# Kernel tuning notes

Hardware: AMD Instinct MI355X
Metric: run time of the kernel (lower is better)

The kernel has to match this reference:

```python
import jax, jax.numpy as jnp
import numpy as np

DIM = 1024
HEAD_NUM = 8
D_HEAD = DIM // HEAD_NUM
B, S = 4, 2048


def setup_inputs() -> dict:
    key = jax.random.key(0)
    ks = jax.random.split(key, 7)
    scale = 0.02
    return {
        "Q": jax.random.normal(ks[0], (B, S, DIM), dtype=jnp.float32),
        "K": jax.random.normal(ks[1], (B, S, DIM), dtype=jnp.float32),
        "V": jax.random.normal(ks[2], (B, S, DIM), dtype=jnp.float32),
        "W_Q": jax.random.normal(ks[3], (DIM, DIM), dtype=jnp.float32) * scale,
        "W_K": jax.random.normal(ks[4], (DIM, DIM), dtype=jnp.float32) * scale,
        "W_V": jax.random.normal(ks[5], (DIM, DIM), dtype=jnp.float32) * scale,
        "W_O": jax.random.normal(ks[6], (DIM, DIM), dtype=jnp.float32) * scale,
    }


def reference(Q, K, V, W_Q, W_K, W_V, W_O):
    # torch nn.Linear(bias=False): y = x @ W.T
    b, s, d = Q.shape
    h, dh = HEAD_NUM, d // HEAD_NUM

    def proj_split(x, W):
        # split_head: tensor_split along feature dim into h contiguous chunks,
        # stack at dim 1 -> [b, h, s, dh]; equivalent to reshape+transpose.
        y = jnp.einsum('bsd,ed->bse', x, W)
        return y.reshape(b, s, h, dh).transpose(0, 2, 1, 3)

    q = proj_split(Q, W_Q)  # [b,h,s,dh]
    k = proj_split(K, W_K)
    v = proj_split(V, W_V)

    scores = jnp.einsum('bhqd,bhkd->bhqk', q, k) / jnp.sqrt(jnp.float32(dh))
    # FAITHFUL to original: nn.Softmax(dim=1) normalizes over the HEAD axis.
    attn = jax.nn.softmax(scores, axis=1)
    # dropout is identity in eval mode
    ctx = jnp.einsum('bhqk,bhkd->bhqd', attn, v)  # [b,h,s,dh]
    # concat_head: heads concatenated back along feature dim in order
    ctx = ctx.transpose(0, 2, 1, 3).reshape(b, s, d)
    return jnp.einsum('bsd,ed->bse', ctx, W_O)
```

## Files before the change

### kernel.cpp

```cpp
#include <hip/hip_runtime.h>
#include <math.h>
#include <stdint.h>


typedef __attribute__((ext_vector_type(8))) __bf16 bf16x8;
typedef __attribute__((ext_vector_type(4))) __bf16 bf16x4;
typedef __attribute__((ext_vector_type(4))) float  f32x4;

__device__ __forceinline__ f32x4 mfma16(bf16x8 a, bf16x8 b, f32x4 c) {
    return __builtin_amdgcn_mfma_f32_16x16x32_bf16(a, b, c, 0, 0, 0);
}

__device__ __forceinline__ void cp16(void* lds, const void* g) {
    __builtin_amdgcn_global_load_lds(
        (__attribute__((address_space(1))) void*)(void*)(const_cast<void*>(g)),
        (__attribute__((address_space(3))) void*)lds,
        16, 0, 0);
}

__global__ void cast_f32_to_bf16(const float* __restrict__ src,
                                 __bf16* __restrict__ dst, int n4) {
    int i = blockIdx.x * blockDim.x + threadIdx.x;
    const int stride = gridDim.x * blockDim.x;
    for (; i < n4; i += stride) {
        float4 f = ((const float4*)src)[i];
        bf16x4 o;
        o[0] = (__bf16)f.x; o[1] = (__bf16)f.y; o[2] = (__bf16)f.z; o[3] = (__bf16)f.w;
        ((bf16x4*)dst)[i] = o;
    }
}

__global__ void cast4_f32_to_bf16(const float* __restrict__ s0, __bf16* __restrict__ d0,
                                  const float* __restrict__ s1, __bf16* __restrict__ d1,
                                  const float* __restrict__ s2, __bf16* __restrict__ d2,
                                  const float* __restrict__ s3, __bf16* __restrict__ d3,
                                  int n4) {
    const float* s = (blockIdx.y == 0) ? s0 : (blockIdx.y == 1) ? s1
                    : (blockIdx.y == 2) ? s2 : s3;
    __bf16* d = (blockIdx.y == 0) ? d0 : (blockIdx.y == 1) ? d1
               : (blockIdx.y == 2) ? d2 : d3;
    int i = blockIdx.x * blockDim.x + threadIdx.x;
    const int stride = gridDim.x * blockDim.x;
    for (; i < n4; i += stride) {
        float4 f = ((const float4*)s)[i];
        bf16x4 o;
        o[0] = (__bf16)f.x; o[1] = (__bf16)f.y; o[2] = (__bf16)f.z; o[3] = (__bf16)f.w;
        ((bf16x4*)d)[i] = o;
    }
}

template<int MODE>
__global__ __launch_bounds__(256, 2) void gemm_bt(const __bf16* __restrict__ A,
                                                  const __bf16* __restrict__ Bt,
                                                  void* __restrict__ out,
                                                  float scale)
{
    __shared__ __bf16 As[128 * 32];
    __shared__ __bf16 Bs[128 * 32];
    const int tid  = threadIdx.x;
    const int lane = tid & 63;
    const int u = lane >> 4, v = lane & 15;
    const int w = tid >> 6;
    const int wm = (w >> 1) * 64, wn = (w & 1) * 64;
    const long tM = (long)blockIdx.y * 128;
    const int  tN = blockIdx.x * 128;

    f32x4 acc[4][4];
#pragma unroll
    for (int i = 0; i < 4; ++i)
#pragma unroll
        for (int j = 0; j < 4; ++j) acc[i][j] = (f32x4){0.f, 0.f, 0.f, 0.f};

    const int c0 = tid, c1 = tid + 256;
    const int ar0 = c0 >> 2, ak0 = (c0 & 3) * 8;
    const int ar1 = c1 >> 2, ak1 = (c1 & 3) * 8;

    const __bf16* Ab = A  + tM * 1024;
    const __bf16* Bb = Bt + (long)tN * 1024;

    for (int k0 = 0; k0 < 1024; k0 += 32) {
        __syncthreads();
        cp16(&As[ar0 * 32 + ak0], Ab + (long)ar0 * 1024 + k0 + ak0);
        cp16(&As[ar1 * 32 + ak1], Ab + (long)ar1 * 1024 + k0 + ak1);
        cp16(&Bs[ar0 * 32 + ak0], Bb + (long)ar0 * 1024 + k0 + ak0);
        cp16(&Bs[ar1 * 32 + ak1], Bb + (long)ar1 * 1024 + k0 + ak1);
        __syncthreads();

        bf16x8 af[4], bfr[4];
#pragma unroll
        for (int i = 0; i < 4; ++i)
            af[i] = *(const bf16x8*)&As[(wm + i * 16 + v) * 32 + u * 8];
#pragma unroll
        for (int j = 0; j < 4; ++j)
            bfr[j] = *(const bf16x8*)&Bs[(wn + j * 16 + v) * 32 + u * 8];
#pragma unroll
        for (int i = 0; i < 4; ++i)
#pragma unroll
            for (int j = 0; j < 4; ++j)
                acc[i][j] = mfma16(af[i], bfr[j], acc[i][j]);
    }

#pragma unroll
    for (int i = 0; i < 4; ++i) {
#pragma unroll
        for (int j = 0; j < 4; ++j) {
            const long row0 = tM + wm + i * 16 + u * 4;
            const int  col  = tN + wn + j * 16 + v;
            if (MODE == 0) {
                __bf16* o = (__bf16*)out;
#pragma unroll
                for (int r = 0; r < 4; ++r)
                    o[(row0 + r) * 1024 + col] = (__bf16)(acc[i][j][r] * scale);
            } else if (MODE == 1) {
                float* o = (float*)out;
#pragma unroll
                for (int r = 0; r < 4; ++r)
                    o[(row0 + r) * 1024 + col] = acc[i][j][r];
            } else {
                __bf16* o = (__bf16*)out;
                const int bidx = (int)(row0 >> 11);
                const int s    = (int)(row0 & 2047);
                const int h = col >> 7, dh = col & 127;
                bf16x4 pk;
#pragma unroll
                for (int r = 0; r < 4; ++r) pk[r] = (__bf16)acc[i][j][r];
                *(bf16x4*)&o[((long)(bidx * 8 + h) * 128 + dh) * 2048 + s] = pk;
            }
        }
    }
}

__global__ __launch_bounds__(256, 4) void qk_head_softmax(
    const __bf16* __restrict__ kp, const __bf16* __restrict__ qp,
    __bf16* __restrict__ P, int b_base, int q_base)
{
    __shared__ __bf16 As[64 * 32];
    __shared__ __bf16 Bs[128 * 32];
    __shared__ __bf16 tb[128 * 68];
    const int tid  = threadIdx.x;
    const int lane = tid & 63;
    const int u = lane >> 4, v = lane & 15;
    const int w = tid >> 6;
    const int wm = (w >> 1) * 32, wn = (w & 1) * 64;
    const int bloc = blockIdx.z;
    const int b    = b_base + bloc;
    const int k0   = blockIdx.x * 64;
    const int q0l  = blockIdx.y * 128;
    const int q0g  = q_base + q0l;
    const long Cq  = (long)gridDim.y * 128;

    const int ar0 = tid >> 2, ak0 = (tid & 3) * 8;
    const int ar1 = ar0 + 64, ak1 = ak0;

    const __bf16* Ka = kp + ((long)b * 2048 + k0) * 1024;
    const __bf16* Qa = qp + ((long)b * 2048 + q0g) * 1024;

    f32x4 den[2][4];
#pragma unroll
    for (int i = 0; i < 2; ++i)
#pragma unroll
        for (int j = 0; j < 4; ++j) den[i][j] = (f32x4){0.f, 0.f, 0.f, 0.f};

#pragma unroll 1
    for (int h = 0; h < 8; ++h) {
        f32x4 acc[2][4];
#pragma unroll
        for (int i = 0; i < 2; ++i)
#pragma unroll
            for (int j = 0; j < 4; ++j) acc[i][j] = (f32x4){0.f, 0.f, 0.f, 0.f};

#pragma unroll
        for (int kb = 0; kb < 4; ++kb) {
            const int co = h * 128 + kb * 32;
            __syncthreads();
            cp16(&As[ar0 * 32 + ak0], Ka + (long)ar0 * 1024 + co + ak0);
            cp16(&Bs[ar0 * 32 + ak0], Qa + (long)ar0 * 1024 + co + ak0);
            cp16(&Bs[ar1 * 32 + ak1], Qa + (long)ar1 * 1024 + co + ak1);
            __syncthreads();

            bf16x8 af[2], bfr[4];
#pragma unroll
            for (int i = 0; i < 2; ++i)
                af[i] = *(const bf16x8*)&As[(wm + i * 16 + v) * 32 + u * 8];
#pragma unroll
            for (int j = 0; j < 4; ++j)
                bfr[j] = *(const bf16x8*)&Bs[(wn + j * 16 + v) * 32 + u * 8];
#pragma unroll
            for (int i = 0; i < 2; ++i)
#pragma unroll
                for (int j = 0; j < 4; ++j)
                    acc[i][j] = mfma16(af[i], bfr[j], acc[i][j]);
        }
#pragma unroll
        for (int i = 0; i < 2; ++i)
#pragma unroll
            for (int j = 0; j < 4; ++j)
#pragma unroll
                for (int r = 0; r < 4; ++r)
                    den[i][j][r] += __expf(acc[i][j][r]);
    }

#pragma unroll
    for (int i = 0; i < 2; ++i)
#pragma unroll
        for (int j = 0; j < 4; ++j)
#pragma unroll
            for (int r = 0; r < 4; ++r) den[i][j][r] = 1.0f / den[i][j][r];

#pragma unroll 1
    for (int h = 0; h < 8; ++h) {
        f32x4 acc[2][4];
#pragma unroll
        for (int i = 0; i < 2; ++i)
#pragma unroll
            for (int j = 0; j < 4; ++j) acc[i][j] = (f32x4){0.f, 0.f, 0.f, 0.f};

#pragma unroll
        for (int kb = 0; kb < 4; ++kb) {
            const int co = h * 128 + kb * 32;
            __syncthreads();
            cp16(&As[ar0 * 32 + ak0], Ka + (long)ar0 * 1024 + co + ak0);
            cp16(&Bs[ar0 * 32 + ak0], Qa + (long)ar0 * 1024 + co + ak0);
            cp16(&Bs[ar1 * 32 + ak1], Qa + (long)ar1 * 1024 + co + ak1);
            __syncthreads();

            bf16x8 af[2], bfr[4];
#pragma unroll
            for (int i = 0; i < 2; ++i)
                af[i] = *(const bf16x8*)&As[(wm + i * 16 + v) * 32 + u * 8];
#pragma unroll
            for (int j = 0; j < 4; ++j)
                bfr[j] = *(const bf16x8*)&Bs[(wn + j * 16 + v) * 32 + u * 8];
#pragma unroll
            for (int i = 0; i < 2; ++i)
#pragma unroll
                for (int j = 0; j < 4; ++j)
                    acc[i][j] = mfma16(af[i], bfr[j], acc[i][j]);
        }
        __syncthreads();
#pragma unroll
        for (int i = 0; i < 2; ++i)
#pragma unroll
            for (int j = 0; j < 4; ++j) {
                const int kc = wm + i * 16 + u * 4;
                const int qr = wn + j * 16 + v;
                bf16x4 o;
#pragma unroll
                for (int r = 0; r < 4; ++r) {
                    float e = (float)(__bf16)__expf(acc[i][j][r]);
                    o[r] = (__bf16)(e * den[i][j][r]);
                }
                *(bf16x4*)&tb[qr * 68 + kc] = o;
            }
        __syncthreads();
        __bf16* Ph = P + ((long)(bloc * 8 + h) * Cq + q0l) * 2048 + k0;
#pragma unroll
        for (int p = 0; p < 4; ++p) {
            const int qq = p * 32 + (tid >> 3);
            const int kk = (tid & 7) * 8;
            *(bf16x8*)&Ph[(long)qq * 2048 + kk] = *(const bf16x8*)&tb[qq * 68 + kk];
        }
    }
}

__global__ __launch_bounds__(256, 2) void pv_gemm(
    const __bf16* __restrict__ vt, const __bf16* __restrict__ P,
    __bf16* __restrict__ ctx, int b_base, int q_base)
{
    __shared__ __bf16 As[128 * 32];
    __shared__ __bf16 Bs[128 * 32];
    const int tid  = threadIdx.x;
    const int lane = tid & 63;
    const int u = lane >> 4, v = lane & 15;
    const int w = tid >> 6;
    const int wm = (w >> 1) * 64, wn = (w & 1) * 64;
    const int bhl  = blockIdx.y;
    const int bloc = bhl >> 3, h = bhl & 7;
    const int b    = b_base + bloc;
    const int q0l  = blockIdx.x * 128;
    const int q0g  = q_base + q0l;
    const long Cq  = (long)gridDim.x * 128;

    const int c0 = tid, c1 = tid + 256;
    const int ar0 = c0 >> 2, ak0 = (c0 & 3) * 8;
    const int ar1 = c1 >> 2, ak1 = (c1 & 3) * 8;

    const __bf16* Ab = vt + (long)(b * 8 + h) * 128 * 2048;
    const __bf16* Bb = P  + ((long)(bloc * 8 + h) * Cq + q0l) * 2048;

    f32x4 acc[4][4];
#pragma unroll
    for (int i = 0; i < 4; ++i)
#pragma unroll
        for (int j = 0; j < 4; ++j) acc[i][j] = (f32x4){0.f, 0.f, 0.f, 0.f};

    for (int k0 = 0; k0 < 2048; k0 += 32) {
        __syncthreads();
        cp16(&As[ar0 * 32 + ak0], Ab + (long)ar0 * 2048 + k0 + ak0);
        cp16(&As[ar1 * 32 + ak1], Ab + (long)ar1 * 2048 + k0 + ak1);
        cp16(&Bs[ar0 * 32 + ak0], Bb + (long)ar0 * 2048 + k0 + ak0);
        cp16(&Bs[ar1 * 32 + ak1], Bb + (long)ar1 * 2048 + k0 + ak1);
        __syncthreads();

        bf16x8 af[4], bfr[4];
#pragma unroll
        for (int i = 0; i < 4; ++i)
            af[i] = *(const bf16x8*)&As[(wm + i * 16 + v) * 32 + u * 8];
#pragma unroll
        for (int j = 0; j < 4; ++j)
            bfr[j] = *(const bf16x8*)&Bs[(wn + j * 16 + v) * 32 + u * 8];
#pragma unroll
        for (int i = 0; i < 4; ++i)
#pragma unroll
            for (int j = 0; j < 4; ++j)
                acc[i][j] = mfma16(af[i], bfr[j], acc[i][j]);
    }

#pragma unroll
    for (int i = 0; i < 4; ++i) {
#pragma unroll
        for (int j = 0; j < 4; ++j) {
            const int dh0 = wm + i * 16 + u * 4;
            const int q   = q0g + wn + j * 16 + v;
            bf16x4 pk;
#pragma unroll
            for (int r = 0; r < 4; ++r) pk[r] = (__bf16)acc[i][j][r];
            *(bf16x4*)&ctx[((long)b * 2048 + q) * 1024 + h * 128 + dh0] = pk;
        }
    }
}

__global__ __launch_bounds__(256, 2) void attn_softmax_head(
    const __bf16* __restrict__ qp, const __bf16* __restrict__ kp,
    const __bf16* __restrict__ vt, __bf16* __restrict__ ctx)
{
    __shared__ float part[8 * 256];
    __shared__ float pb[4][2][16 * 33];

    const int tid  = threadIdx.x;
    const int lane = tid & 63;
    const int w = tid >> 6;
    const int u = lane >> 4, v = lane & 15;
    const int b  = blockIdx.y;
    const int q0 = blockIdx.x * 16;

    const long qoff = ((long)b * 2048 + q0 + v) * 1024;
    bf16x8 qf[2][4];
#pragma unroll
    for (int hh = 0; hh < 2; ++hh) {
        const int h = 2 * w + hh;
#pragma unroll
        for (int kk = 0; kk < 4; ++kk)
            qf[hh][kk] = *(const bf16x8*)(qp + qoff + h * 128 + kk * 32 + u * 8);
    }

    f32x4 acc[2][8];
#pragma unroll
    for (int hh = 0; hh < 2; ++hh)
#pragma unroll
        for (int dt = 0; dt < 8; ++dt) acc[hh][dt] = (f32x4){0.f, 0.f, 0.f, 0.f};

    for (int kt = 0; kt < 2048; kt += 32) {
        float e[2][2][4];
#pragma unroll
        for (int hh = 0; hh < 2; ++hh) {
            const int h = 2 * w + hh;
#pragma unroll
            for (int t = 0; t < 2; ++t) {
                f32x4 s = (f32x4){0.f, 0.f, 0.f, 0.f};
                const __bf16* kb = kp + ((long)b * 2048 + kt + t * 16 + v) * 1024
                                      + h * 128 + u * 8;
#pragma unroll
                for (int kk = 0; kk < 4; ++kk)
                    s = mfma16(*(const bf16x8*)(kb + kk * 32), qf[hh][kk], s);
#pragma unroll
                for (int r = 0; r < 4; ++r) e[hh][t][r] = __expf(s[r]);
            }
        }
#pragma unroll
        for (int t = 0; t < 2; ++t)
#pragma unroll
            for (int r = 0; r < 4; ++r)
                part[(t * 4 + r) * 256 + w * 64 + lane] = e[0][t][r] + e[1][t][r];
        __syncthreads();
#pragma unroll
        for (int t = 0; t < 2; ++t)
#pragma unroll
            for (int r = 0; r < 4; ++r) {
                const int j = (t * 4 + r) * 256 + lane;
                const float den = part[j] + part[j + 64] + part[j + 128] + part[j + 192];
                const float rinv = 1.0f / den;
                const int kl = t * 16 + u * 4 + r;
                pb[w][0][v * 33 + kl] = e[0][t][r] * rinv;
                pb[w][1][v * 33 + kl] = e[1][t][r] * rinv;
            }
        bf16x8 pf[2];
#pragma unroll
        for (int hh = 0; hh < 2; ++hh)
#pragma unroll
            for (int jj = 0; jj < 8; ++jj)
                pf[hh][jj] = (__bf16)pb[w][hh][v * 33 + u * 8 + jj];
#pragma unroll
        for (int hh = 0; hh < 2; ++hh) {
            const int h = 2 * w + hh;
            const __bf16* vb = vt + ((long)(b * 8 + h) * 128 + v) * 2048 + kt + u * 8;
#pragma unroll
            for (int dt = 0; dt < 8; ++dt)
                acc[hh][dt] = mfma16(*(const bf16x8*)(vb + (long)dt * 16 * 2048),
                                     pf[hh], acc[hh][dt]);
        }
        __syncthreads();
    }

#pragma unroll
    for (int hh = 0; hh < 2; ++hh) {
        const int h = 2 * w + hh;
#pragma unroll
        for (int dt = 0; dt < 8; ++dt) {
            bf16x4 o;
#pragma unroll
            for (int r = 0; r < 4; ++r) o[r] = (__bf16)acc[hh][dt][r];
            *(bf16x4*)(ctx + ((long)b * 2048 + q0 + v) * 1024
                           + h * 128 + dt * 16 + u * 4) = o;
        }
    }
}

extern "C" void kernel_launch(void* const* d_in, const int* in_sizes, int n_in,
                              void* d_out, int out_size, void* d_ws, size_t ws_size,
                              hipStream_t stream)
{
    const float* Q  = (const float*)d_in[0];
    const float* K  = (const float*)d_in[1];
    const float* V  = (const float*)d_in[2];
    const float* WQ = (const float*)d_in[3];
    const float* WK = (const float*)d_in[4];
    const float* WV = (const float*)d_in[5];
    const float* WO = (const float*)d_in[6];

    __bf16* ws = (__bf16*)d_ws;
    __bf16* wq = ws;
    __bf16* wk = wq + 1048576;
    __bf16* wv = wk + 1048576;
    __bf16* wo = wv + 1048576;
    __bf16* xb = wo + 1048576;
    __bf16* qp = xb + 8388608;
    __bf16* kp = qp + 8388608;
    __bf16* vt = kp + 8388608;
    __bf16* pbuf = vt + 8388608;

    const float qscale = 0.08838834764831845f;

    cast4_f32_to_bf16<<<dim3(256, 4), 256, 0, stream>>>(
        WQ, wq, WK, wk, WV, wv, WO, wo, 262144);

    dim3 gg(8, 64), gb(256);
    cast_f32_to_bf16<<<4096, 256, 0, stream>>>(Q, xb, 2097152);
    gemm_bt<0><<<gg, gb, 0, stream>>>(xb, wq, qp, qscale);
    cast_f32_to_bf16<<<4096, 256, 0, stream>>>(K, xb, 2097152);
    gemm_bt<0><<<gg, gb, 0, stream>>>(xb, wk, kp, 1.0f);
    cast_f32_to_bf16<<<4096, 256, 0, stream>>>(V, xb, 2097152);
    gemm_bt<2><<<gg, gb, 0, stream>>>(xb, wv, vt, 1.0f);

    const size_t baseBytes = 37748736ULL * 2ULL;
    const size_t avail = (ws_size > baseBytes) ? ws_size - baseBytes : 0;
    const int cfgs[6][2] = {{4,2048},{2,2048},{1,2048},{1,1024},{1,512},{1,256}};
    int nb = 0, C = 0;
    for (int c = 0; c < 6; ++c) {
        const size_t need = (size_t)cfgs[c][0] * 8 * cfgs[c][1] * 2048 * 2;
        if (need <= avail) { nb = cfgs[c][0]; C = cfgs[c][1]; break; }
    }

    if (nb) {
        for (int bb = 0; bb < 4; bb += nb)
            for (int qq = 0; qq < 2048; qq += C) {
                qk_head_softmax<<<dim3(32, C / 128, nb), gb, 0, stream>>>(
                    kp, qp, pbuf, bb, qq);
                pv_gemm<<<dim3(C / 128, nb * 8), gb, 0, stream>>>(
                    vt, pbuf, xb, bb, qq);
            }
    } else {
        attn_softmax_head<<<dim3(128, 4), gb, 0, stream>>>(qp, kp, vt, xb);
    }

    gemm_bt<1><<<gg, gb, 0, stream>>>(xb, wo, (float*)d_out, 1.0f);
}
```

Baseline: 502.1 us.

## Fuse head-axis softmax and PV into one attention kernel; batch QKV projections

Replaces the materialized probability buffer path (qk_head_softmax writing P, then pv_gemm) with a single fused_attn kernel. In it, eight waves each own one head for a 32-query tile, the softmax denominator across heads is reduced through LDS, and the normalized probabilities are fed straight into the PV MFMAs. The three input casts and the three projection GEMMs are each batched into single launches via a grid z/y dimension. This removes the large P round trip through HBM and several launches. In exchange, K and V are read directly from global memory without LDS tiling, and the kernel needs two block-wide syncs per key tile.

```diff
diff --git a/kernel.cpp b/kernel.cpp
--- a/kernel.cpp
+++ b/kernel.cpp
@@ -16,18 +16,6 @@
         (__attribute__((address_space(1))) void*)(void*)(const_cast<void*>(g)),
         (__attribute__((address_space(3))) void*)lds,
         16, 0, 0);
-}
-
-__global__ void cast_f32_to_bf16(const float* __restrict__ src,
-                                 __bf16* __restrict__ dst, int n4) {
-    int i = blockIdx.x * blockDim.x + threadIdx.x;
-    const int stride = gridDim.x * blockDim.x;
-    for (; i < n4; i += stride) {
-        float4 f = ((const float4*)src)[i];
-        bf16x4 o;
-        o[0] = (__bf16)f.x; o[1] = (__bf16)f.y; o[2] = (__bf16)f.z; o[3] = (__bf16)f.w;
-        ((bf16x4*)dst)[i] = o;
-    }
 }
 
 __global__ void cast4_f32_to_bf16(const float* __restrict__ s0, __bf16* __restrict__ d0,
@@ -49,6 +37,22 @@
     }
 }
 
+__global__ void cast3_f32_to_bf16(const float* __restrict__ s0, __bf16* __restrict__ d0,
+                                  const float* __restrict__ s1, __bf16* __restrict__ d1,
+                                  const float* __restrict__ s2, __bf16* __restrict__ d2,
+                                  int n4) {
+    const float* s = (blockIdx.y == 0) ? s0 : (blockIdx.y == 1) ? s1 : s2;
+    __bf16* d = (blockIdx.y == 0) ? d0 : (blockIdx.y == 1) ? d1 : d2;
+    int i = blockIdx.x * blockDim.x + threadIdx.x;
+    const int stride = gridDim.x * blockDim.x;
+    for (; i < n4; i += stride) {
+        float4 f = ((const float4*)s)[i];
+        bf16x4 o;
+        o[0] = (__bf16)f.x; o[1] = (__bf16)f.y; o[2] = (__bf16)f.z; o[3] = (__bf16)f.w;
+        ((bf16x4*)d)[i] = o;
+    }
+}
+
 template<int MODE>
 __global__ __launch_bounds__(256, 2) void gemm_bt(const __bf16* __restrict__ A,
                                                   const __bf16* __restrict__ Bt,
@@ -106,200 +110,64 @@
         for (int j = 0; j < 4; ++j) {
             const long row0 = tM + wm + i * 16 + u * 4;
             const int  col  = tN + wn + j * 16 + v;
-            if (MODE == 0) {
-                __bf16* o = (__bf16*)out;
-#pragma unroll
-                for (int r = 0; r < 4; ++r)
-                    o[(row0 + r) * 1024 + col] = (__bf16)(acc[i][j][r] * scale);
-            } else if (MODE == 1) {
+            if (MODE == 1) {
                 float* o = (float*)out;
 #pragma unroll
                 for (int r = 0; r < 4; ++r)
                     o[(row0 + r) * 1024 + col] = acc[i][j][r];
             } else {
                 __bf16* o = (__bf16*)out;
-                const int bidx = (int)(row0 >> 11);
-                const int s    = (int)(row0 & 2047);
-                const int h = col >> 7, dh = col & 127;
-                bf16x4 pk;
-#pragma unroll
-                for (int r = 0; r < 4; ++r) pk[r] = (__bf16)acc[i][j][r];
-                *(bf16x4*)&o[((long)(bidx * 8 + h) * 128 + dh) * 2048 + s] = pk;
+#pragma unroll
+                for (int r = 0; r < 4; ++r)
+                    o[(row0 + r) * 1024 + col] = (__bf16)(acc[i][j][r] * scale);
             }
         }
     }
 }
 
-__global__ __launch_bounds__(256, 4) void qk_head_softmax(
-    const __bf16* __restrict__ kp, const __bf16* __restrict__ qp,
-    __bf16* __restrict__ P, int b_base, int q_base)
-{
-    __shared__ __bf16 As[64 * 32];
-    __shared__ __bf16 Bs[128 * 32];
-    __shared__ __bf16 tb[128 * 68];
-    const int tid  = threadIdx.x;
-    const int lane = tid & 63;
-    const int u = lane >> 4, v = lane & 15;
-    const int w = tid >> 6;
-    const int wm = (w >> 1) * 32, wn = (w & 1) * 64;
-    const int bloc = blockIdx.z;
-    const int b    = b_base + bloc;
-    const int k0   = blockIdx.x * 64;
-    const int q0l  = blockIdx.y * 128;
-    const int q0g  = q_base + q0l;
-    const long Cq  = (long)gridDim.y * 128;
-
-    const int ar0 = tid >> 2, ak0 = (tid & 3) * 8;
-    const int ar1 = ar0 + 64, ak1 = ak0;
-
-    const __bf16* Ka = kp + ((long)b * 2048 + k0) * 1024;
-    const __bf16* Qa = qp + ((long)b * 2048 + q0g) * 1024;
-
-    f32x4 den[2][4];
-#pragma unroll
-    for (int i = 0; i < 2; ++i)
-#pragma unroll
-        for (int j = 0; j < 4; ++j) den[i][j] = (f32x4){0.f, 0.f, 0.f, 0.f};
-
-#pragma unroll 1
-    for (int h = 0; h < 8; ++h) {
-        f32x4 acc[2][4];
-#pragma unroll
-        for (int i = 0; i < 2; ++i)
-#pragma unroll
-            for (int j = 0; j < 4; ++j) acc[i][j] = (f32x4){0.f, 0.f, 0.f, 0.f};
-
-#pragma unroll
-        for (int kb = 0; kb < 4; ++kb) {
-            const int co = h * 128 + kb * 32;
-            __syncthreads();
-            cp16(&As[ar0 * 32 + ak0], Ka + (long)ar0 * 1024 + co + ak0);
-            cp16(&Bs[ar0 * 32 + ak0], Qa + (long)ar0 * 1024 + co + ak0);
-            cp16(&Bs[ar1 * 32 + ak1], Qa + (long)ar1 * 1024 + co + ak1);
-            __syncthreads();
-
-            bf16x8 af[2], bfr[4];
-#pragma unroll
-            for (int i = 0; i < 2; ++i)
-                af[i] = *(const bf16x8*)&As[(wm + i * 16 + v) * 32 + u * 8];
-#pragma unroll
-            for (int j = 0; j < 4; ++j)
-                bfr[j] = *(const bf16x8*)&Bs[(wn + j * 16 + v) * 32 + u * 8];
-#pragma unroll
-            for (int i = 0; i < 2; ++i)
-#pragma unroll
-                for (int j = 0; j < 4; ++j)
-                    acc[i][j] = mfma16(af[i], bfr[j], acc[i][j]);
-        }
-#pragma unroll
-        for (int i = 0; i < 2; ++i)
-#pragma unroll
-            for (int j = 0; j < 4; ++j)
-#pragma unroll
-                for (int r = 0; r < 4; ++r)
-                    den[i][j][r] += __expf(acc[i][j][r]);
-    }
-
-#pragma unroll
-    for (int i = 0; i < 2; ++i)
-#pragma unroll
-        for (int j = 0; j < 4; ++j)
-#pragma unroll
-            for (int r = 0; r < 4; ++r) den[i][j][r] = 1.0f / den[i][j][r];
-
-#pragma unroll 1
-    for (int h = 0; h < 8; ++h) {
-        f32x4 acc[2][4];
-#pragma unroll
-        for (int i = 0; i < 2; ++i)
-#pragma unroll
-            for (int j = 0; j < 4; ++j) acc[i][j] = (f32x4){0.f, 0.f, 0.f, 0.f};
-
-#pragma unroll
-        for (int kb = 0; kb < 4; ++kb) {
-            const int co = h * 128 + kb * 32;
-            __syncthreads();
-            cp16(&As[ar0 * 32 + ak0], Ka + (long)ar0 * 1024 + co + ak0);
-            cp16(&Bs[ar0 * 32 + ak0], Qa + (long)ar0 * 1024 + co + ak0);
-            cp16(&Bs[ar1 * 32 + ak1], Qa + (long)ar1 * 1024 + co + ak1);
-            __syncthreads();
-
-            bf16x8 af[2], bfr[4];
-#pragma unroll
-            for (int i = 0; i < 2; ++i)
-                af[i] = *(const bf16x8*)&As[(wm + i * 16 + v) * 32 + u * 8];
-#pragma unroll
-            for (int j = 0; j < 4; ++j)
-                bfr[j] = *(const bf16x8*)&Bs[(wn + j * 16 + v) * 32 + u * 8];
-#pragma unroll
-            for (int i = 0; i < 2; ++i)
-#pragma unroll
-                for (int j = 0; j < 4; ++j)
-                    acc[i][j] = mfma16(af[i], bfr[j], acc[i][j]);
-        }
-        __syncthreads();
-#pragma unroll
-        for (int i = 0; i < 2; ++i)
-#pragma unroll
-            for (int j = 0; j < 4; ++j) {
-                const int kc = wm + i * 16 + u * 4;
-                const int qr = wn + j * 16 + v;
-                bf16x4 o;
-#pragma unroll
-                for (int r = 0; r < 4; ++r) {
-                    float e = (float)(__bf16)__expf(acc[i][j][r]);
-                    o[r] = (__bf16)(e * den[i][j][r]);
-                }
-                *(bf16x4*)&tb[qr * 68 + kc] = o;
-            }
-        __syncthreads();
-        __bf16* Ph = P + ((long)(bloc * 8 + h) * Cq + q0l) * 2048 + k0;
-#pragma unroll
-        for (int p = 0; p < 4; ++p) {
-            const int qq = p * 32 + (tid >> 3);
-            const int kk = (tid & 7) * 8;
-            *(bf16x8*)&Ph[(long)qq * 2048 + kk] = *(const bf16x8*)&tb[qq * 68 + kk];
-        }
-    }
-}
-
-__global__ __launch_bounds__(256, 2) void pv_gemm(
-    const __bf16* __restrict__ vt, const __bf16* __restrict__ P,
-    __bf16* __restrict__ ctx, int b_base, int q_base)
+__global__ __launch_bounds__(256, 2) void qkv_proj(
+    const __bf16* __restrict__ xq, const __bf16* __restrict__ xk,
+    const __bf16* __restrict__ xv,
+    const __bf16* __restrict__ wq, const __bf16* __restrict__ wk,
+    const __bf16* __restrict__ wv,
+    __bf16* __restrict__ qp, __bf16* __restrict__ kp, __bf16* __restrict__ vtb,
+    float qscale)
 {
     __shared__ __bf16 As[128 * 32];
     __shared__ __bf16 Bs[128 * 32];
+    const int z = blockIdx.z;
+    const __bf16* A  = (z == 0) ? xq : (z == 1) ? xk : xv;
+    const __bf16* Bt = (z == 0) ? wq : (z == 1) ? wk : wv;
+    __bf16* out      = (z == 0) ? qp : (z == 1) ? kp : vtb;
+    const float scale = (z == 0) ? qscale : 1.0f;
+
     const int tid  = threadIdx.x;
     const int lane = tid & 63;
     const int u = lane >> 4, v = lane & 15;
     const int w = tid >> 6;
     const int wm = (w >> 1) * 64, wn = (w & 1) * 64;
-    const int bhl  = blockIdx.y;
-    const int bloc = bhl >> 3, h = bhl & 7;
-    const int b    = b_base + bloc;
-    const int q0l  = blockIdx.x * 128;
-    const int q0g  = q_base + q0l;
-    const long Cq  = (long)gridDim.x * 128;
+    const long tM = (long)blockIdx.y * 128;
+    const int  tN = blockIdx.x * 128;
+
+    f32x4 acc[4][4];
+#pragma unroll
+    for (int i = 0; i < 4; ++i)
+#pragma unroll
+        for (int j = 0; j < 4; ++j) acc[i][j] = (f32x4){0.f, 0.f, 0.f, 0.f};
 
     const int c0 = tid, c1 = tid + 256;
     const int ar0 = c0 >> 2, ak0 = (c0 & 3) * 8;
     const int ar1 = c1 >> 2, ak1 = (c1 & 3) * 8;
 
-    const __bf16* Ab = vt + (long)(b * 8 + h) * 128 * 2048;
-    const __bf16* Bb = P  + ((long)(bloc * 8 + h) * Cq + q0l) * 2048;
-
-    f32x4 acc[4][4];
-#pragma unroll
-    for (int i = 0; i < 4; ++i)
-#pragma unroll
-        for (int j = 0; j < 4; ++j) acc[i][j] = (f32x4){0.f, 0.f, 0.f, 0.f};
-
-    for (int k0 = 0; k0 < 2048; k0 += 32) {
-        __syncthreads();
-        cp16(&As[ar0 * 32 + ak0], Ab + (long)ar0 * 2048 + k0 + ak0);
-        cp16(&As[ar1 * 32 + ak1], Ab + (long)ar1 * 2048 + k0 + ak1);
-        cp16(&Bs[ar0 * 32 + ak0], Bb + (long)ar0 * 2048 + k0 + ak0);
-        cp16(&Bs[ar1 * 32 + ak1], Bb + (long)ar1 * 2048 + k0 + ak1);
+    const __bf16* Ab = A  + tM * 1024;
+    const __bf16* Bb = Bt + (long)tN * 1024;
+
+    for (int k0 = 0; k0 < 1024; k0 += 32) {
+        __syncthreads();
+        cp16(&As[ar0 * 32 + ak0], Ab + (long)ar0 * 1024 + k0 + ak0);
+        cp16(&As[ar1 * 32 + ak1], Ab + (long)ar1 * 1024 + k0 + ak1);
+        cp16(&Bs[ar0 * 32 + ak0], Bb + (long)ar0 * 1024 + k0 + ak0);
+        cp16(&Bs[ar1 * 32 + ak1], Bb + (long)ar1 * 1024 + k0 + ak1);
         __syncthreads();
 
         bf16x8 af[4], bfr[4];
@@ -320,110 +188,159 @@
     for (int i = 0; i < 4; ++i) {
 #pragma unroll
         for (int j = 0; j < 4; ++j) {
-            const int dh0 = wm + i * 16 + u * 4;
-            const int q   = q0g + wn + j * 16 + v;
-            bf16x4 pk;
-#pragma unroll
-            for (int r = 0; r < 4; ++r) pk[r] = (__bf16)acc[i][j][r];
-            *(bf16x4*)&ctx[((long)b * 2048 + q) * 1024 + h * 128 + dh0] = pk;
-        }
-    }
-}
-
-__global__ __launch_bounds__(256, 2) void attn_softmax_head(
+            const long row0 = tM + wm + i * 16 + u * 4;
+            const int  col  = tN + wn + j * 16 + v;
+            if (z < 2) {
+#pragma unroll
+                for (int r = 0; r < 4; ++r)
+                    out[(row0 + r) * 1024 + col] = (__bf16)(acc[i][j][r] * scale);
+            } else {
+                const int bidx = (int)(row0 >> 11);
+                const int s    = (int)(row0 & 2047);
+                const int h = col >> 7, dh = col & 127;
+                bf16x4 pk;
+#pragma unroll
+                for (int r = 0; r < 4; ++r) pk[r] = (__bf16)acc[i][j][r];
+                *(bf16x4*)&out[((long)(bidx * 8 + h) * 128 + dh) * 2048 + s] = pk;
+            }
+        }
+    }
+}
+
+__global__ __launch_bounds__(512, 2) void fused_attn(
     const __bf16* __restrict__ qp, const __bf16* __restrict__ kp,
     const __bf16* __restrict__ vt, __bf16* __restrict__ ctx)
 {
-    __shared__ float part[8 * 256];
-    __shared__ float pb[4][2][16 * 33];
+    __shared__ f32x4 dbuf[8][8][64];
+    __shared__ f32x4 rbuf[8][64];
+    __shared__ __bf16 Pl[8][32][64];
 
     const int tid  = threadIdx.x;
+    const int w    = tid >> 6;
     const int lane = tid & 63;
-    const int w = tid >> 6;
     const int u = lane >> 4, v = lane & 15;
-    const int b  = blockIdx.y;
-    const int q0 = blockIdx.x * 16;
-
-    const long qoff = ((long)b * 2048 + q0 + v) * 1024;
+
+    const int g0 = blockIdx.x;
+    const int xs = g0 & 7, idx = g0 >> 3;
+    const int b  = xs >> 1;
+    const int qt = idx * 2 + (xs & 1);
+    const int q0 = qt * 32;
+    const int h  = w;
+
+    const __bf16* Qb = qp + ((long)b * 2048 + q0) * 1024 + h * 128;
+    const __bf16* Kb = kp + (long)b * 2048 * 1024 + h * 128;
+    const __bf16* Vb = vt + (long)(b * 8 + h) * 128 * 2048;
+
     bf16x8 qf[2][4];
 #pragma unroll
-    for (int hh = 0; hh < 2; ++hh) {
-        const int h = 2 * w + hh;
+    for (int qj = 0; qj < 2; ++qj)
 #pragma unroll
         for (int kk = 0; kk < 4; ++kk)
-            qf[hh][kk] = *(const bf16x8*)(qp + qoff + h * 128 + kk * 32 + u * 8);
-    }
-
-    f32x4 acc[2][8];
-#pragma unroll
-    for (int hh = 0; hh < 2; ++hh)
-#pragma unroll
-        for (int dt = 0; dt < 8; ++dt) acc[hh][dt] = (f32x4){0.f, 0.f, 0.f, 0.f};
-
-    for (int kt = 0; kt < 2048; kt += 32) {
-        float e[2][2][4];
-#pragma unroll
-        for (int hh = 0; hh < 2; ++hh) {
-            const int h = 2 * w + hh;
-#pragma unroll
-            for (int t = 0; t < 2; ++t) {
-                f32x4 s = (f32x4){0.f, 0.f, 0.f, 0.f};
-                const __bf16* kb = kp + ((long)b * 2048 + kt + t * 16 + v) * 1024
-                                      + h * 128 + u * 8;
+            qf[qj][kk] = *(const bf16x8*)&Qb[(long)(qj * 16 + v) * 1024 + kk * 32 + u * 8];
+
+    f32x4 ctxa[8][2];
+#pragma unroll
+    for (int dt = 0; dt < 8; ++dt)
+#pragma unroll
+        for (int qj = 0; qj < 2; ++qj) ctxa[dt][qj] = (f32x4){0.f, 0.f, 0.f, 0.f};
+
+    for (int kt = 0; kt < 2048; kt += 64) {
+        f32x4 e[4][2];
+#pragma unroll
+        for (int ki = 0; ki < 4; ++ki)
+#pragma unroll
+            for (int qj = 0; qj < 2; ++qj) e[ki][qj] = (f32x4){0.f, 0.f, 0.f, 0.f};
+
+#pragma unroll
+        for (int ki = 0; ki < 4; ++ki) {
+            bf16x8 kf[4];
+#pragma unroll
+            for (int kk = 0; kk < 4; ++kk)
+                kf[kk] = *(const bf16x8*)&Kb[(long)(kt + ki * 16 + v) * 1024 + kk * 32 + u * 8];
+#pragma unroll
+            for (int qj = 0; qj < 2; ++qj)
 #pragma unroll
                 for (int kk = 0; kk < 4; ++kk)
-                    s = mfma16(*(const bf16x8*)(kb + kk * 32), qf[hh][kk], s);
-#pragma unroll
-                for (int r = 0; r < 4; ++r) e[hh][t][r] = __expf(s[r]);
+                    e[ki][qj] = mfma16(kf[kk], qf[qj][kk], e[ki][qj]);
+        }
+
+#pragma unroll
+        for (int ki = 0; ki < 4; ++ki)
+#pragma unroll
+            for (int qj = 0; qj < 2; ++qj)
+#pragma unroll
+                for (int r = 0; r < 4; ++r)
+                    e[ki][qj][r] = __expf(e[ki][qj][r]);
+
+        bf16x8 vf0[8];
+#pragma unroll
+        for (int dt = 0; dt < 8; ++dt)
+            vf0[dt] = *(const bf16x8*)&Vb[(long)(dt * 16 + v) * 2048 + kt + u * 8];
+
+#pragma unroll
+        for (int ki = 0; ki < 4; ++ki)
+#pragma unroll
+            for (int qj = 0; qj < 2; ++qj)
+                dbuf[w][ki * 2 + qj][lane] = e[ki][qj];
+        __syncthreads();
+
+        f32x4 d = dbuf[0][w][lane];
+#pragma unroll
+        for (int wp = 1; wp < 8; ++wp) {
+            f32x4 t = dbuf[wp][w][lane];
+#pragma unroll
+            for (int r = 0; r < 4; ++r) d[r] += t[r];
+        }
+        f32x4 rv;
+#pragma unroll
+        for (int r = 0; r < 4; ++r) rv[r] = 1.0f / d[r];
+        rbuf[w][lane] = rv;
+        __syncthreads();
+
+#pragma unroll
+        for (int ki = 0; ki < 4; ++ki)
+#pragma unroll
+            for (int qj = 0; qj < 2; ++qj) {
+                f32x4 rr = rbuf[ki * 2 + qj][lane];
+                bf16x4 o;
+#pragma unroll
+                for (int r = 0; r < 4; ++r) o[r] = (__bf16)(e[ki][qj][r] * rr[r]);
+                const int q  = qj * 16 + v;
+                const int ch = (ki * 2 + (u >> 1)) ^ (v & 7);
+                *(bf16x4*)((char*)&Pl[w][q][0] + ch * 16 + (u & 1) * 8) = o;
             }
-        }
-#pragma unroll
-        for (int t = 0; t < 2; ++t)
-#pragma unroll
-            for (int r = 0; r < 4; ++r)
-                part[(t * 4 + r) * 256 + w * 64 + lane] = e[0][t][r] + e[1][t][r];
-        __syncthreads();
-#pragma unroll
-        for (int t = 0; t < 2; ++t)
-#pragma unroll
-            for (int r = 0; r < 4; ++r) {
-                const int j = (t * 4 + r) * 256 + lane;
-                const float den = part[j] + part[j + 64] + part[j + 128] + part[j + 192];
-                const float rinv = 1.0f / den;
-                const int kl = t * 16 + u * 4 + r;
-                pb[w][0][v * 33 + kl] = e[0][t][r] * rinv;
-                pb[w][1][v * 33 + kl] = e[1][t][r] * rinv;
+
+        bf16x8 pfr[2][2];
+#pragma unroll
+        for (int kc = 0; kc < 2; ++kc)
+#pragma unroll
+            for (int qj = 0; qj < 2; ++qj) {
+                const int q  = qj * 16 + v;
+                const int ch = (kc * 4 + u) ^ (v & 7);
+                pfr[kc][qj] = *(const bf16x8*)((const char*)&Pl[w][q][0] + ch * 16);
             }
-        bf16x8 pf[2];
-#pragma unroll
-        for (int hh = 0; hh < 2; ++hh)
-#pragma unroll
-            for (int jj = 0; jj < 8; ++jj)
-                pf[hh][jj] = (__bf16)pb[w][hh][v * 33 + u * 8 + jj];
-#pragma unroll
-        for (int hh = 0; hh < 2; ++hh) {
-            const int h = 2 * w + hh;
-            const __bf16* vb = vt + ((long)(b * 8 + h) * 128 + v) * 2048 + kt + u * 8;
-#pragma unroll
-            for (int dt = 0; dt < 8; ++dt)
-                acc[hh][dt] = mfma16(*(const bf16x8*)(vb + (long)dt * 16 * 2048),
-                                     pf[hh], acc[hh][dt]);
-        }
-        __syncthreads();
-    }
-
-#pragma unroll
-    for (int hh = 0; hh < 2; ++hh) {
-        const int h = 2 * w + hh;
 #pragma unroll
         for (int dt = 0; dt < 8; ++dt) {
+#pragma unroll
+            for (int qj = 0; qj < 2; ++qj)
+                ctxa[dt][qj] = mfma16(vf0[dt], pfr[0][qj], ctxa[dt][qj]);
+            bf16x8 vf1 = *(const bf16x8*)&Vb[(long)(dt * 16 + v) * 2048 + kt + 32 + u * 8];
+#pragma unroll
+            for (int qj = 0; qj < 2; ++qj)
+                ctxa[dt][qj] = mfma16(vf1, pfr[1][qj], ctxa[dt][qj]);
+        }
+    }
+
+#pragma unroll
+    for (int dt = 0; dt < 8; ++dt)
+#pragma unroll
+        for (int qj = 0; qj < 2; ++qj) {
             bf16x4 o;
 #pragma unroll
-            for (int r = 0; r < 4; ++r) o[r] = (__bf16)acc[hh][dt][r];
-            *(bf16x4*)(ctx + ((long)b * 2048 + q0 + v) * 1024
-                           + h * 128 + dt * 16 + u * 4) = o;
-        }
-    }
+            for (int r = 0; r < 4; ++r) o[r] = (__bf16)ctxa[dt][qj][r];
+            *(bf16x4*)&ctx[((long)b * 2048 + q0 + qj * 16 + v) * 1024
+                           + h * 128 + dt * 16 + u * 4] = o;
+        }
 }
 
 extern "C" void kernel_launch(void* const* d_in, const int* in_sizes, int n_in,
@@ -443,45 +360,24 @@
     __bf16* wk = wq + 1048576;
     __bf16* wv = wk + 1048576;
     __bf16* wo = wv + 1048576;
-    __bf16* xb = wo + 1048576;
-    __bf16* qp = xb + 8388608;
+    __bf16* xq = wo + 1048576;
+    __bf16* xk = xq + 8388608;
+    __bf16* xv = xk + 8388608;
+    __bf16* qp = xv + 8388608;
     __bf16* kp = qp + 8388608;
     __bf16* vt = kp + 8388608;
-    __bf16* pbuf = vt + 8388608;
+    __bf16* xb = vt + 8388608;
 
     const float qscale = 0.08838834764831845f;
 
     cast4_f32_to_bf16<<<dim3(256, 4), 256, 0, stream>>>(
         WQ, wq, WK, wk, WV, wv, WO, wo, 262144);
-
-    dim3 gg(8, 64), gb(256);
-    cast_f32_to_bf16<<<4096, 256, 0, stream>>>(Q, xb, 2097152);
-    gemm_bt<0><<<gg, gb, 0, stream>>>(xb, wq, qp, qscale);
-    cast_f32_to_bf16<<<4096, 256, 0, stream>>>(K, xb, 2097152);
-    gemm_bt<0><<<gg, gb, 0, stream>>>(xb, wk, kp, 1.0f);
-    cast_f32_to_bf16<<<4096, 256, 0, stream>>>(V, xb, 2097152);
-    gemm_bt<2><<<gg, gb, 0, stream>>>(xb, wv, vt, 1.0f);
-
-    const size_t baseBytes = 37748736ULL * 2ULL;
-    const size_t avail = (ws_size > baseBytes) ? ws_size - baseBytes : 0;
-    const int cfgs[6][2] = {{4,2048},{2,2048},{1,2048},{1,1024},{1,512},{1,256}};
-    int nb = 0, C = 0;
-    for (int c = 0; c < 6; ++c) {
-        const size_t need = (size_t)cfgs[c][0] * 8 * cfgs[c][1] * 2048 * 2;
-        if (need <= avail) { nb = cfgs[c][0]; C = cfgs[c][1]; break; }
-    }
-
-    if (nb) {
-        for (int bb = 0; bb < 4; bb += nb)
-            for (int qq = 0; qq < 2048; qq += C) {
-                qk_head_softmax<<<dim3(32, C / 128, nb), gb, 0, stream>>>(
-                    kp, qp, pbuf, bb, qq);
-                pv_gemm<<<dim3(C / 128, nb * 8), gb, 0, stream>>>(
-                    vt, pbuf, xb, bb, qq);
-            }
-    } else {
-        attn_softmax_head<<<dim3(128, 4), gb, 0, stream>>>(qp, kp, vt, xb);
-    }
-
-    gemm_bt<1><<<gg, gb, 0, stream>>>(xb, wo, (float*)d_out, 1.0f);
-}
+    cast3_f32_to_bf16<<<dim3(2048, 3), 256, 0, stream>>>(
+        Q, xq, K, xk, V, xv, 2097152);
+    qkv_proj<<<dim3(8, 64, 3), 256, 0, stream>>>(
+        xq, xk, xv, wq, wk, wv, qp, kp, vt, qscale);
+
+    fused_attn<<<256, 512, 0, stream>>>(qp, kp, vt, xb);
+
+    gemm_bt<1><<<dim3(8, 64), 256, 0, stream>>>(xb, wo, (float*)d_out, 1.0f);
+}
```

Result: no change. 510.3 us (+1.6%).
